# Kernel tuning notes

Hardware: AMD Instinct MI355X
Metric: run time of the kernel (lower is better)

## Reference

```python
import jax, jax.numpy as jnp
import numpy as np

B, N, T, D, H, E = 2, 1024, 8, 128, 4, 8192
DH = D // H
NEG_SLOPE = 0.2  # GATv2Conv default negative_slope


def _ln(x, g, b):
    m = jnp.mean(x, -1, keepdims=True)
    v = jnp.mean((x - m) ** 2, -1, keepdims=True)
    return (x - m) * jax.lax.rsqrt(v + 1e-5) * g + b


def _forward(x, edge_index, gat_wl, gat_wr, gat_att, gat_b, in_w, in_b, out_w, out_b,
             ffn_w1, ffn_b1, ffn_w2, ffn_b2, fus_w, fus_b,
             lns_g, lns_b, lnt1_g, lnt1_b, lnt2_g, lnt2_b, lnf_g, lnf_b):
    # ---- spatial branch: GATv2, vectorized over (B, T) instead of python loops ----
    loops = jnp.arange(N)
    src = jnp.concatenate([edge_index[0], loops])  # j: message source (PyG adds self loops)
    dst = jnp.concatenate([edge_index[1], loops])  # i: aggregation target
    xl = jnp.einsum('bntd,de->bnte', x, gat_wl).reshape(B, N, T, H, D)
    xr = jnp.einsum('bntd,de->bnte', x, gat_wr).reshape(B, N, T, H, D)
    ml = xl[:, src]                                  # [B,Et,T,H,D]
    mr = xr[:, dst]
    e = jax.nn.leaky_relu(ml + mr, NEG_SLOPE)
    logits = jnp.einsum('bethd,hd->beth', e, gat_att)
    logits = jnp.moveaxis(logits, 1, 0)              # [Et,B,T,H]
    mx = jax.ops.segment_max(logits, dst, num_segments=N)
    p = jnp.exp(logits - mx[dst])                    # stable edge softmax per dst node
    ssum = jax.ops.segment_sum(p, dst, num_segments=N)
    alpha = p / ssum[dst]                            # [Et,B,T,H]
    msg = alpha[..., None] * jnp.moveaxis(ml, 1, 0)
    agg = jax.ops.segment_sum(msg, dst, num_segments=N)  # [N,B,T,H,D]
    x_sp = jnp.moveaxis(agg.mean(3), 0, 1) + gat_b   # concat=False -> head mean; [B,N,T,D]
    x_sp = _ln(x_sp, lns_g, lns_b)

    # ---- temporal branch: MHA + FFN, vectorized over all B*N nodes ----
    xt = x.reshape(B * N, T, D)
    qkv = xt @ in_w + in_b
    q, k, v = jnp.split(qkv, 3, axis=-1)
    q = q.reshape(B * N, T, H, DH)
    k = k.reshape(B * N, T, H, DH)
    v = v.reshape(B * N, T, H, DH)
    scores = jnp.einsum('bthd,bshd->bhts', q, k) / np.float32(np.sqrt(DH))
    attn = jax.nn.softmax(scores, -1)
    o = jnp.einsum('bhts,bshd->bthd', attn, v).reshape(B * N, T, D)
    o = o @ out_w + out_b
    x1 = _ln(xt + o, lnt1_g, lnt1_b)
    ffn = jax.nn.gelu(x1 @ ffn_w1 + ffn_b1, approximate=False) @ ffn_w2 + ffn_b2
    x_tp = _ln(x1 + ffn, lnt2_g, lnt2_b).reshape(B, N, T, D)

    # ---- gated fusion with residual ----
    g = jax.nn.sigmoid(jnp.concatenate([x_sp, x_tp], -1) @ fus_w + fus_b)
    return _ln(g * x_sp + (1.0 - g) * x_tp + x, lnf_g, lnf_b)


def setup_inputs() -> dict:
    key = jax.random.key(0)
    ks = jax.random.split(key, 12)
    s = 0.05
    f = jnp.float32
    return {
        'x': jax.random.normal(ks[0], (B, N, T, D), f),
        'edge_index': jax.random.randint(ks[1], (2, E), 0, N),
        'gat_wl': jax.random.normal(ks[2], (D, H * D), f) * s,
        'gat_wr': jax.random.normal(ks[3], (D, H * D), f) * s,
        'gat_att': jax.random.normal(ks[4], (H, D), f) * s,
        'gat_b': jnp.zeros((D,), f),
        'in_w': jax.random.normal(ks[5], (D, 3 * D), f) * s,
        'in_b': jnp.zeros((3 * D,), f),
        'out_w': jax.random.normal(ks[6], (D, D), f) * s,
        'out_b': jnp.zeros((D,), f),
        'ffn_w1': jax.random.normal(ks[7], (D, 4 * D), f) * s,
        'ffn_b1': jnp.zeros((4 * D,), f),
        'ffn_w2': jax.random.normal(ks[8], (4 * D, D), f) * s,
        'ffn_b2': jnp.zeros((D,), f),
        'fus_w': jax.random.normal(ks[9], (2 * D, D), f) * s,
        'fus_b': jnp.zeros((D,), f),
        'lns_g': jnp.ones((D,), f), 'lns_b': jnp.zeros((D,), f),
        'lnt1_g': jnp.ones((D,), f), 'lnt1_b': jnp.zeros((D,), f),
        'lnt2_g': jnp.ones((D,), f), 'lnt2_b': jnp.zeros((D,), f),
        'lnf_g': jnp.ones((D,), f), 'lnf_b': jnp.zeros((D,), f),
    }


def reference(x, edge_index, gat_wl, gat_wr, gat_att, gat_b, in_w, in_b, out_w, out_b,
              ffn_w1, ffn_b1, ffn_w2, ffn_b2, fus_w, fus_b,
              lns_g, lns_b, lnt1_g, lnt1_b, lnt2_g, lnt2_b, lnf_g, lnf_b):
    return _forward(x, edge_index, gat_wl, gat_wr, gat_att, gat_b, in_w, in_b, out_w, out_b,
                    ffn_w1, ffn_b1, ffn_w2, ffn_b2, fus_w, fus_b,
                    lns_g, lns_b, lnt1_g, lnt1_b, lnt2_g, lnt2_b, lnf_g, lnf_b)
```

## Files before the change

kernel.cpp:

```cpp
#include <hip/hip_runtime.h>
#include <math.h>

#define B_ 2
#define N_ 1024
#define T_ 8
#define D_ 128
#define H_ 4
#define E_ 8192
#define EN_ 9216
#define M_ 16384

typedef unsigned short u16;
using bf16x8 = __attribute__((ext_vector_type(8))) short;
using f32x4  = __attribute__((ext_vector_type(4))) float;

__device__ __forceinline__ float bf2f(unsigned int u) {
  return __uint_as_float(u << 16);
}
__device__ __forceinline__ u16 f2bf(float f) {
  unsigned int x = __float_as_uint(f);
  x += 0x7fffu + ((x >> 16) & 1u);
  return (u16)(x >> 16);
}
__device__ __forceinline__ void load8f(const u16* p, float* f) {
  uint4 u = *(const uint4*)p;
  f[0]=bf2f(u.x & 0xffffu); f[1]=bf2f(u.x >> 16);
  f[2]=bf2f(u.y & 0xffffu); f[3]=bf2f(u.y >> 16);
  f[4]=bf2f(u.z & 0xffffu); f[5]=bf2f(u.z >> 16);
  f[6]=bf2f(u.w & 0xffffu); f[7]=bf2f(u.w >> 16);
}
__device__ __forceinline__ void unpack8(uint4 u, float* f) {
  f[0]=bf2f(u.x & 0xffffu); f[1]=bf2f(u.x >> 16);
  f[2]=bf2f(u.y & 0xffffu); f[3]=bf2f(u.y >> 16);
  f[4]=bf2f(u.z & 0xffffu); f[5]=bf2f(u.z >> 16);
  f[6]=bf2f(u.w & 0xffffu); f[7]=bf2f(u.w >> 16);
}
__device__ __forceinline__ void gl2lds(const u16* g, u16* l) {
  __builtin_amdgcn_global_load_lds(
      (const __attribute__((address_space(1))) unsigned int*)(const void*)g,
      (__attribute__((address_space(3))) unsigned int*)(void*)l,
      16, 0, 0);
}

__device__ __forceinline__ u16 conv_w_elem(int idx,
    const float* wl, const float* wr, const float* inw, const float* outw,
    const float* f1, const float* f2, const float* fw) {
  const float* src; int base, K, N;
  if      (idx < 65536)  { src = wl;   base = 0;      K = 128; N = 512; }
  else if (idx < 131072) { src = wr;   base = 65536;  K = 128; N = 512; }
  else if (idx < 180224) { src = inw;  base = 131072; K = 128; N = 384; }
  else if (idx < 196608) { src = outw; base = 180224; K = 128; N = 128; }
  else if (idx < 262144) { src = f1;   base = 196608; K = 128; N = 512; }
  else if (idx < 327680) { src = f2;   base = 262144; K = 512; N = 128; }
  else                   { src = fw;   base = 327680; K = 256; N = 128; }
  int o = idx - base;
  int n = o / K, k = o - n * K;
  return f2bf(src[k * N + n]);
}

__global__ __launch_bounds__(1024) void prep_csr_k(const float* __restrict__ x,
    const float* __restrict__ wl, const float* __restrict__ wr,
    const float* __restrict__ inw, const float* __restrict__ outw,
    const float* __restrict__ f1, const float* __restrict__ f2,
    const float* __restrict__ fw,
    u16* __restrict__ XB, u16* __restrict__ WB,
    const int* __restrict__ ei, int* __restrict__ offs, int* __restrict__ srcs) {
  __shared__ int cnt[N_];
  __shared__ int cur[N_];
  int bi = blockIdx.x;
  int tid = threadIdx.x;
  if (bi < 512) {
    int i = (bi * 1024 + tid) * 4;
    float4 v = *(const float4*)&x[i];
    u16 o[4] = {f2bf(v.x), f2bf(v.y), f2bf(v.z), f2bf(v.w)};
    *(ushort4*)&XB[i] = *(ushort4*)o;
    return;
  }
  if (bi < 600) {
    int base = (bi - 512) * 4096 + tid * 4;
#pragma unroll
    for (int j = 0; j < 4; ++j)
      WB[base + j] = conv_w_elem(base + j, wl, wr, inw, outw, f1, f2, fw);
    return;
  }
  cnt[tid] = 0;
  __syncthreads();
  for (int e = tid; e < EN_; e += 1024) {
    int d = (e < E_) ? ei[E_ + e] : (e - E_);
    atomicAdd(&cnt[d], 1);
  }
  __syncthreads();
  int mine = cnt[tid];
  for (int off = 1; off < 1024; off <<= 1) {
    int tv = (tid >= off) ? cnt[tid - off] : 0;
    __syncthreads();
    cnt[tid] += tv;
    __syncthreads();
  }
  int excl = cnt[tid] - mine;
  offs[tid] = excl;
  if (tid == 1023) offs[N_] = cnt[1023];
  cur[tid] = excl;
  __syncthreads();
  for (int e = tid; e < EN_; e += 1024) {
    int d = (e < E_) ? ei[E_ + e] : (e - E_);
    int s = (e < E_) ? ei[e] : (e - E_);
    int pos = atomicAdd(&cur[d], 1);
    srcs[pos] = s;
  }
}

template<int BM, int ACT, int ROUTE>
__global__ __launch_bounds__(256) void gemm_k(const u16* __restrict__ A, int lda,
                                              const u16* __restrict__ WT, int K,
                                              const float* __restrict__ bias,
                                              u16* __restrict__ C, int ldc,
                                              u16* __restrict__ R0,
                                              u16* __restrict__ R1,
                                              u16* __restrict__ R2,
                                              const float* __restrict__ b2) {
  constexpr int MI = BM / 32;
  __shared__ u16 As[BM * 32];
  __shared__ u16 Bs[128 * 32];
  int tid = threadIdx.x;
  int bx = blockIdx.x, by = blockIdx.y;
  int lane = tid & 63, wid = tid >> 6;
  int lr = lane & 15, lk = lane >> 4;
  int wm = (wid >> 1) * (BM / 2);
  int wn = (wid & 1) * 64;

  u16* Cb; int ldc_; int col0; const float* bias_;
  if (ROUTE) {
    if (bx < 4)      { Cb = R0; ldc_ = 512; col0 = bx * 128;       bias_ = nullptr; }
    else if (bx < 8) { Cb = R1; ldc_ = 512; col0 = (bx - 4) * 128; bias_ = nullptr; }
    else             { Cb = R2; ldc_ = 384; col0 = (bx - 8) * 128; bias_ = b2; }
  } else { Cb = C; ldc_ = ldc; col0 = bx * 128; bias_ = bias; }

  f32x4 acc[MI][4] = {};
  for (int k0 = 0; k0 < K; k0 += 32) {
    __syncthreads();
#pragma unroll
    for (int i = 0; i < BM / 64; ++i) {
      int o = tid * 16 + i * 4096;
      int row = o >> 6;
      int col = (o >> 1) & 31;
      gl2lds(A + (size_t)(by * BM + row) * lda + k0 + col,
             (u16*)((char*)As + wid * 1024 + i * 4096));
    }
#pragma unroll
    for (int i = 0; i < 2; ++i) {
      int o = tid * 16 + i * 4096;
      int nrow = o >> 6;
      int col = (o >> 1) & 31;
      gl2lds(WT + (size_t)(bx * 128 + nrow) * K + k0 + col,
             (u16*)((char*)Bs + wid * 1024 + i * 4096));
    }
    __syncthreads();
    bf16x8 bf[4];
#pragma unroll
    for (int ni = 0; ni < 4; ++ni)
      bf[ni] = *(const bf16x8*)&Bs[(wn + ni * 16 + lr) * 32 + lk * 8];
#pragma unroll
    for (int mi = 0; mi < MI; ++mi) {
      bf16x8 af = *(const bf16x8*)&As[(wm + mi * 16 + lr) * 32 + lk * 8];
#pragma unroll
      for (int ni = 0; ni < 4; ++ni)
        acc[mi][ni] = __builtin_amdgcn_mfma_f32_16x16x32_bf16(af, bf[ni], acc[mi][ni], 0, 0, 0);
    }
  }
  float bc[4];
#pragma unroll
  for (int ni = 0; ni < 4; ++ni)
    bc[ni] = bias_ ? bias_[col0 + wn + ni * 16 + lr] : 0.f;
#pragma unroll
  for (int mi = 0; mi < MI; ++mi) {
#pragma unroll
    for (int r = 0; r < 4; ++r) {
      int row = by * BM + wm + mi * 16 + lk * 4 + r;
#pragma unroll
      for (int ni = 0; ni < 4; ++ni) {
        int col = col0 + wn + ni * 16 + lr;
        float v = acc[mi][ni][r] + bc[ni];
        if (ACT) v = 0.5f * v * (1.f + erff(v * 0.70710678118f));
        Cb[(size_t)row * ldc_ + col] = f2bf(v);
      }
    }
  }
}

template<int EPI>
__global__ __launch_bounds__(256) void gemm_ln_k(const u16* __restrict__ A, int lda,
                                                 const u16* __restrict__ WT, int K,
                                                 const float* __restrict__ bias,
                                                 const float* __restrict__ xres,
                                                 const u16* __restrict__ xcat,
                                                 const float* __restrict__ lng,
                                                 const float* __restrict__ lnb,
                                                 float* __restrict__ o32,
                                                 u16* __restrict__ o16, int os16) {
  __shared__ u16 As[64 * 32];
  __shared__ u16 Bs[128 * 32];
  __shared__ float rs[64][2], rq[64][2];
  int tid = threadIdx.x;
  int by = blockIdx.y;
  int lane = tid & 63, wid = tid >> 6;
  int lr = lane & 15, lk = lane >> 4;
  int wm = (wid >> 1) * 32, wn = (wid & 1) * 64;

  f32x4 acc[2][4] = {};
  for (int k0 = 0; k0 < K; k0 += 32) {
    __syncthreads();
    {
      int o = tid * 16;
      int row = o >> 6;
      int col = (o >> 1) & 31;
      gl2lds(A + (size_t)(by * 64 + row) * lda + k0 + col,
             (u16*)((char*)As + wid * 1024));
    }
#pragma unroll
    for (int i = 0; i < 2; ++i) {
      int o = tid * 16 + i * 4096;
      int nrow = o >> 6;
      int col = (o >> 1) & 31;
      gl2lds(WT + (size_t)nrow * K + k0 + col,
             (u16*)((char*)Bs + wid * 1024 + i * 4096));
    }
    __syncthreads();
    bf16x8 bf[4];
#pragma unroll
    for (int ni = 0; ni < 4; ++ni)
      bf[ni] = *(const bf16x8*)&Bs[(wn + ni * 16 + lr) * 32 + lk * 8];
#pragma unroll
    for (int mi = 0; mi < 2; ++mi) {
      bf16x8 af = *(const bf16x8*)&As[(wm + mi * 16 + lr) * 32 + lk * 8];
#pragma unroll
      for (int ni = 0; ni < 4; ++ni)
        acc[mi][ni] = __builtin_amdgcn_mfma_f32_16x16x32_bf16(af, bf[ni], acc[mi][ni], 0, 0, 0);
    }
  }
  float bc[4];
#pragma unroll
  for (int ni = 0; ni < 4; ++ni) bc[ni] = bias[wn + ni * 16 + lr];

#pragma unroll
  for (int mi = 0; mi < 2; ++mi) {
#pragma unroll
    for (int r = 0; r < 4; ++r) {
      int row = by * 64 + wm + mi * 16 + lk * 4 + r;
      float s = 0.f, s2 = 0.f;
#pragma unroll
      for (int ni = 0; ni < 4; ++ni) {
        int col = wn + ni * 16 + lr;
        float v = acc[mi][ni][r] + bc[ni];
        if (EPI == 1 || EPI == 2) {
          v += xres[(size_t)row * 128 + col];
        } else {
          float gg = 1.f / (1.f + __expf(-v));
          float xsp = bf2f(xcat[(size_t)row * 256 + col]);
          float xtp = bf2f(xcat[(size_t)row * 256 + 128 + col]);
          v = gg * xsp + (1.f - gg) * xtp + xres[(size_t)row * 128 + col];
        }
        acc[mi][ni][r] = v;
        s += v; s2 += v * v;
      }
      s += __shfl_xor(s, 1, 64); s2 += __shfl_xor(s2, 1, 64);
      s += __shfl_xor(s, 2, 64); s2 += __shfl_xor(s2, 2, 64);
      s += __shfl_xor(s, 4, 64); s2 += __shfl_xor(s2, 4, 64);
      s += __shfl_xor(s, 8, 64); s2 += __shfl_xor(s2, 8, 64);
      if (lr == 0) {
        int rl = wm + mi * 16 + lk * 4 + r;
        rs[rl][wid & 1] = s;
        rq[rl][wid & 1] = s2;
      }
    }
  }
  __syncthreads();
#pragma unroll
  for (int mi = 0; mi < 2; ++mi) {
#pragma unroll
    for (int r = 0; r < 4; ++r) {
      int rl = wm + mi * 16 + lk * 4 + r;
      int row = by * 64 + rl;
      float tot = rs[rl][0] + rs[rl][1];
      float tq = rq[rl][0] + rq[rl][1];
      float mean = tot * (1.f / 128.f);
      float var = tq * (1.f / 128.f) - mean * mean;
      float rinv = rsqrtf(var + 1e-5f);
#pragma unroll
      for (int ni = 0; ni < 4; ++ni) {
        int col = wn + ni * 16 + lr;
        float o = (acc[mi][ni][r] - mean) * rinv * lng[col] + lnb[col];
        if (EPI != 2) o32[(size_t)row * 128 + col] = o;
        if (EPI != 3) o16[(size_t)row * os16 + col] = f2bf(o);
      }
    }
  }
}

__global__ __launch_bounds__(256) void gat_attn_k(const u16* __restrict__ XL,
                                                  const u16* __restrict__ XR,
                                                  const int* __restrict__ offs,
                                                  const int* __restrict__ srcs,
                                                  const float* __restrict__ att,
                                                  const float* __restrict__ gb,
                                                  const float* __restrict__ lng,
                                                  const float* __restrict__ lnb,
                                                  u16* __restrict__ XCAT,
                                                  const u16* __restrict__ QKV,
                                                  u16* __restrict__ OATT) {
  int bid = blockIdx.x;
  int wid = threadIdx.x >> 6;
  int lane = threadIdx.x & 63;
  if (bid < 4096) {
    int w = bid * 4 + wid;
    int n = w >> 4;
    int b = (w >> 3) & 1;
    int t = w & 7;
    int dd = (lane & 15) * 8;
    size_t tokn = (size_t)(b * N_ + n) * 8 + t;
    size_t rowoff = (size_t)b * (N_ * 8) + t;

    float mr[8], av[8];
    load8f(XR + tokn * 512 + lane * 8, mr);
    *(float4*)&av[0] = *(const float4*)(att + lane * 8);
    *(float4*)&av[4] = *(const float4*)(att + lane * 8 + 4);

    int beg = offs[n], end = offs[n + 1];
    float sH = 0.f;
    float acc[8] = {0.f, 0.f, 0.f, 0.f, 0.f, 0.f, 0.f, 0.f};
    int src0 = srcs[beg];
    uint4 raw_next = *(const uint4*)(XL + (rowoff + (size_t)src0 * 8) * 512 + lane * 8);
    for (int i = beg; i < end; ++i) {
      uint4 raw = raw_next;
      if (i + 1 < end) {
        int sn = srcs[i + 1];
        raw_next = *(const uint4*)(XL + (rowoff + (size_t)sn * 8) * 512 + lane * 8);
      }
      float ml[8];
      unpack8(raw, ml);
      float d = 0.f;
#pragma unroll
      for (int j = 0; j < 8; ++j) {
        float m = ml[j] + mr[j];
        m = fmaxf(m, 0.2f * m);
        d += m * av[j];
      }
      d += __shfl_xor(d, 1, 64);
      d += __shfl_xor(d, 2, 64);
      d += __shfl_xor(d, 4, 64);
      d += __shfl_xor(d, 8, 64);
      float p = __expf(d);
      sH += p;
#pragma unroll
      for (int j = 0; j < 8; ++j) acc[j] += p * ml[j];
    }
    float invS = 1.f / sH;
#pragma unroll
    for (int j = 0; j < 8; ++j) acc[j] *= invS;
#pragma unroll
    for (int j = 0; j < 8; ++j) {
      acc[j] += __shfl_xor(acc[j], 16, 64);
      acc[j] += __shfl_xor(acc[j], 32, 64);
    }
#pragma unroll
    for (int j = 0; j < 8; ++j) acc[j] = acc[j] * 0.25f + gb[dd + j];
    float s = 0.f, s2 = 0.f;
#pragma unroll
    for (int j = 0; j < 8; ++j) { s += acc[j]; s2 += acc[j] * acc[j]; }
#pragma unroll
    for (int m = 1; m < 16; m <<= 1) {
      s += __shfl_xor(s, m, 64);
      s2 += __shfl_xor(s2, m, 64);
    }
    float mean = s * (1.f / 128.f);
    float var = s2 * (1.f / 128.f) - mean * mean;
    float r = rsqrtf(var + 1e-5f);
    if (lane < 16) {
      u16 ob[8];
#pragma unroll
      for (int j = 0; j < 8; ++j)
        ob[j] = f2bf((acc[j] - mean) * r * lng[dd + j] + lnb[dd + j]);
      *(uint4*)&XCAT[tokn * 256 + dd] = *(uint4*)ob;
    }
    return;
  }
  int pair = (bid - 4096) * 4 + wid;
  int bn = pair >> 2, h = pair & 3;
  int t = lane >> 3, sidx = lane & 7;
  int dg = lane & 7;
  const u16* base = QKV + (size_t)bn * 8 * 384;
  float va[8][4];
#pragma unroll
  for (int s2 = 0; s2 < 8; ++s2) {
    ushort4 vv = *(const ushort4*)(base + s2 * 384 + 256 + h * 32 + dg * 4);
    va[s2][0] = bf2f(vv.x); va[s2][1] = bf2f(vv.y);
    va[s2][2] = bf2f(vv.z); va[s2][3] = bf2f(vv.w);
  }
  const u16* qp = base + t * 384 + h * 32;
  const u16* kp = base + sidx * 384 + 128 + h * 32;
  float sc = 0.f;
#pragma unroll
  for (int d0 = 0; d0 < 32; d0 += 8) {
    float q[8], k[8];
    load8f(qp + d0, q);
    load8f(kp + d0, k);
#pragma unroll
    for (int j = 0; j < 8; ++j) sc += q[j] * k[j];
  }
  sc *= 0.17677669529663687f;
  float m = sc;
  m = fmaxf(m, __shfl_xor(m, 1, 64));
  m = fmaxf(m, __shfl_xor(m, 2, 64));
  m = fmaxf(m, __shfl_xor(m, 4, 64));
  float p = __expf(sc - m);
  float S = p;
  S += __shfl_xor(S, 1, 64);
  S += __shfl_xor(S, 2, 64);
  S += __shfl_xor(S, 4, 64);
  float alpha = p / S;
  int tbase = lane & 56;
  float o0 = 0.f, o1 = 0.f, o2 = 0.f, o3 = 0.f;
#pragma unroll
  for (int s2 = 0; s2 < 8; ++s2) {
    float a = __shfl(alpha, tbase + s2, 64);
    o0 += a * va[s2][0];
    o1 += a * va[s2][1];
    o2 += a * va[s2][2];
    o3 += a * va[s2][3];
  }
  u16 ov[4] = {f2bf(o0), f2bf(o1), f2bf(o2), f2bf(o3)};
  *(ushort4*)&OATT[((size_t)bn * 8 + t) * 128 + h * 32 + dg * 4] = *(ushort4*)ov;
}

extern "C" void kernel_launch(void* const* d_in, const int* in_sizes, int n_in,
                              void* d_out, int out_size, void* d_ws, size_t ws_size,
                              hipStream_t stream) {
  const float* x       = (const float*)d_in[0];
  const int*   ei      = (const int*)d_in[1];
  const float* gat_att = (const float*)d_in[4];
  const float* gat_b   = (const float*)d_in[5];
  const float* in_b    = (const float*)d_in[7];
  const float* out_b   = (const float*)d_in[9];
  const float* ffn_b1  = (const float*)d_in[11];
  const float* ffn_b2  = (const float*)d_in[13];
  const float* fus_b   = (const float*)d_in[15];
  const float* lns_g   = (const float*)d_in[16];
  const float* lns_b   = (const float*)d_in[17];
  const float* lnt1_g  = (const float*)d_in[18];
  const float* lnt1_b  = (const float*)d_in[19];
  const float* lnt2_g  = (const float*)d_in[20];
  const float* lnt2_b  = (const float*)d_in[21];
  const float* lnf_g   = (const float*)d_in[22];
  const float* lnf_b   = (const float*)d_in[23];

  char* ws = (char*)d_ws;
  u16*   WB    = (u16*)ws;
  u16*   WT1   = WB;
  u16*   WTO   = WB + 180224;
  u16*   WTF1  = WB + 196608;
  u16*   WTF2  = WB + 262144;
  u16*   WTFUS = WB + 327680;
  int*   OFFS  = (int*)(ws + 3145728);
  int*   SRCS  = (int*)(ws + 3153920);
  u16*   XB   = (u16*)(ws + 4194304);
  u16*   OATT = XB;
  u16*   XL   = (u16*)(ws + 8388608);
  u16*   FFNH = XL;
  u16*   XR   = (u16*)(ws + 25165824);
  float* X1   = (float*)(ws + 33554432);
  u16*   QKV  = (u16*)(ws + 41943040);
  u16*   X1B  = (u16*)(ws + 41943040);
  u16*   XCAT = (u16*)(ws + 62914560);

  prep_csr_k<<<dim3(601), dim3(1024), 0, stream>>>(x,
      (const float*)d_in[2], (const float*)d_in[3], (const float*)d_in[6],
      (const float*)d_in[8], (const float*)d_in[10], (const float*)d_in[12],
      (const float*)d_in[14], XB, WB, ei, OFFS, SRCS);

  gemm_k<128,0,1><<<dim3(11, 128), dim3(256), 0, stream>>>(
      XB, 128, WT1, 128, nullptr, nullptr, 0, XL, XR, QKV, in_b);

  gat_attn_k<<<dim3(6144), dim3(256), 0, stream>>>(XL, XR, OFFS, SRCS,
      gat_att, gat_b, lns_g, lns_b, XCAT, QKV, OATT);

  gemm_ln_k<1><<<dim3(1, 256), dim3(256), 0, stream>>>(
      OATT, 128, WTO, 128, out_b, x, nullptr, lnt1_g, lnt1_b, X1, X1B, 128);

  gemm_k<128,1,0><<<dim3(4, 128), dim3(256), 0, stream>>>(
      X1B, 128, WTF1, 128, ffn_b1, FFNH, 512, nullptr, nullptr, nullptr, nullptr);

  gemm_ln_k<2><<<dim3(1, 256), dim3(256), 0, stream>>>(
      FFNH, 512, WTF2, 512, ffn_b2, X1, nullptr, lnt2_g, lnt2_b,
      nullptr, XCAT + 128, 256);

  gemm_ln_k<3><<<dim3(1, 256), dim3(256), 0, stream>>>(
      XCAT, 256, WTFUS, 256, fus_b, x, XCAT, lnf_g, lnf_b,
      (float*)d_out, nullptr, 0);
}
```

Baseline: 223.2 us.

## Fuse all stages into one persistent kernel with software grid barriers

Replaces seven separate kernel launches with a single persistent kernel of 768 blocks that loops over virtual tiles for each stage and separates stages with atomic-counter grid barriers. The aim is to remove launch overhead and inter-kernel gaps between the short stages. In exchange, it relies on all 768 blocks being co-resident (launch bounds of 3 blocks per CU), which risks deadlock if occupancy is lower. It also adds barrier spin cost and does CSR construction in a single 256-thread block.

```diff
diff --git a/kernel.cpp b/kernel.cpp
--- a/kernel.cpp
+++ b/kernel.cpp
@@ -9,6 +9,7 @@
 #define E_ 8192
 #define EN_ 9216
 #define M_ 16384
+#define G_ 768
 
 typedef unsigned short u16;
 using bf16x8 = __attribute__((ext_vector_type(8))) short;
@@ -40,6 +41,17 @@
       (const __attribute__((address_space(1))) unsigned int*)(const void*)g,
       (__attribute__((address_space(3))) unsigned int*)(void*)l,
       16, 0, 0);
+}
+
+__device__ __forceinline__ void gridbar(int* bar, int idx) {
+  __syncthreads();
+  if (threadIdx.x == 0) {
+    __threadfence();
+    atomicAdd(&bar[idx], 1);
+    while (atomicAdd(&bar[idx], 0) < G_) __builtin_amdgcn_s_sleep(1);
+    __threadfence();
+  }
+  __syncthreads();
 }
 
 __device__ __forceinline__ u16 conv_w_elem(int idx,
@@ -58,72 +70,13 @@
   return f2bf(src[k * N + n]);
 }
 
-__global__ __launch_bounds__(1024) void prep_csr_k(const float* __restrict__ x,
-    const float* __restrict__ wl, const float* __restrict__ wr,
-    const float* __restrict__ inw, const float* __restrict__ outw,
-    const float* __restrict__ f1, const float* __restrict__ f2,
-    const float* __restrict__ fw,
-    u16* __restrict__ XB, u16* __restrict__ WB,
-    const int* __restrict__ ei, int* __restrict__ offs, int* __restrict__ srcs) {
-  __shared__ int cnt[N_];
-  __shared__ int cur[N_];
-  int bi = blockIdx.x;
+template<int BM, int ACT, int ROUTE>
+__device__ __forceinline__ void gemm_tile(int bx, int by,
+    const u16* A, int lda, const u16* WT, int K, const float* bias,
+    u16* C, int ldc, u16* R0, u16* R1, u16* R2, const float* b2,
+    u16* As, u16* Bs) {
+  constexpr int MI = BM / 32;
   int tid = threadIdx.x;
-  if (bi < 512) {
-    int i = (bi * 1024 + tid) * 4;
-    float4 v = *(const float4*)&x[i];
-    u16 o[4] = {f2bf(v.x), f2bf(v.y), f2bf(v.z), f2bf(v.w)};
-    *(ushort4*)&XB[i] = *(ushort4*)o;
-    return;
-  }
-  if (bi < 600) {
-    int base = (bi - 512) * 4096 + tid * 4;
-#pragma unroll
-    for (int j = 0; j < 4; ++j)
-      WB[base + j] = conv_w_elem(base + j, wl, wr, inw, outw, f1, f2, fw);
-    return;
-  }
-  cnt[tid] = 0;
-  __syncthreads();
-  for (int e = tid; e < EN_; e += 1024) {
-    int d = (e < E_) ? ei[E_ + e] : (e - E_);
-    atomicAdd(&cnt[d], 1);
-  }
-  __syncthreads();
-  int mine = cnt[tid];
-  for (int off = 1; off < 1024; off <<= 1) {
-    int tv = (tid >= off) ? cnt[tid - off] : 0;
-    __syncthreads();
-    cnt[tid] += tv;
-    __syncthreads();
-  }
-  int excl = cnt[tid] - mine;
-  offs[tid] = excl;
-  if (tid == 1023) offs[N_] = cnt[1023];
-  cur[tid] = excl;
-  __syncthreads();
-  for (int e = tid; e < EN_; e += 1024) {
-    int d = (e < E_) ? ei[E_ + e] : (e - E_);
-    int s = (e < E_) ? ei[e] : (e - E_);
-    int pos = atomicAdd(&cur[d], 1);
-    srcs[pos] = s;
-  }
-}
-
-template<int BM, int ACT, int ROUTE>
-__global__ __launch_bounds__(256) void gemm_k(const u16* __restrict__ A, int lda,
-                                              const u16* __restrict__ WT, int K,
-                                              const float* __restrict__ bias,
-                                              u16* __restrict__ C, int ldc,
-                                              u16* __restrict__ R0,
-                                              u16* __restrict__ R1,
-                                              u16* __restrict__ R2,
-                                              const float* __restrict__ b2) {
-  constexpr int MI = BM / 32;
-  __shared__ u16 As[BM * 32];
-  __shared__ u16 Bs[128 * 32];
-  int tid = threadIdx.x;
-  int bx = blockIdx.x, by = blockIdx.y;
   int lane = tid & 63, wid = tid >> 6;
   int lr = lane & 15, lk = lane >> 4;
   int wm = (wid >> 1) * (BM / 2);
@@ -189,20 +142,12 @@
 }
 
 template<int EPI>
-__global__ __launch_bounds__(256) void gemm_ln_k(const u16* __restrict__ A, int lda,
-                                                 const u16* __restrict__ WT, int K,
-                                                 const float* __restrict__ bias,
-                                                 const float* __restrict__ xres,
-                                                 const u16* __restrict__ xcat,
-                                                 const float* __restrict__ lng,
-                                                 const float* __restrict__ lnb,
-                                                 float* __restrict__ o32,
-                                                 u16* __restrict__ o16, int os16) {
-  __shared__ u16 As[64 * 32];
-  __shared__ u16 Bs[128 * 32];
-  __shared__ float rs[64][2], rq[64][2];
+__device__ __forceinline__ void gemm_ln_tile(int by,
+    const u16* A, int lda, const u16* WT, int K, const float* bias,
+    const float* xres, const u16* xcat, const float* lng, const float* lnb,
+    float* o32, u16* o16, int os16,
+    u16* As, u16* Bs, float* rs, float* rq) {
   int tid = threadIdx.x;
-  int by = blockIdx.y;
   int lane = tid & 63, wid = tid >> 6;
   int lr = lane & 15, lk = lane >> 4;
   int wm = (wid >> 1) * 32, wn = (wid & 1) * 64;
@@ -269,8 +214,8 @@
       s += __shfl_xor(s, 8, 64); s2 += __shfl_xor(s2, 8, 64);
       if (lr == 0) {
         int rl = wm + mi * 16 + lk * 4 + r;
-        rs[rl][wid & 1] = s;
-        rq[rl][wid & 1] = s2;
+        rs[rl * 2 + (wid & 1)] = s;
+        rq[rl * 2 + (wid & 1)] = s2;
       }
     }
   }
@@ -281,8 +226,8 @@
     for (int r = 0; r < 4; ++r) {
       int rl = wm + mi * 16 + lk * 4 + r;
       int row = by * 64 + rl;
-      float tot = rs[rl][0] + rs[rl][1];
-      float tq = rq[rl][0] + rq[rl][1];
+      float tot = rs[rl * 2] + rs[rl * 2 + 1];
+      float tq = rq[rl * 2] + rq[rl * 2 + 1];
       float mean = tot * (1.f / 128.f);
       float var = tq * (1.f / 128.f) - mean * mean;
       float rinv = rsqrtf(var + 1e-5f);
@@ -295,96 +240,86 @@
       }
     }
   }
-}
-
-__global__ __launch_bounds__(256) void gat_attn_k(const u16* __restrict__ XL,
-                                                  const u16* __restrict__ XR,
-                                                  const int* __restrict__ offs,
-                                                  const int* __restrict__ srcs,
-                                                  const float* __restrict__ att,
-                                                  const float* __restrict__ gb,
-                                                  const float* __restrict__ lng,
-                                                  const float* __restrict__ lnb,
-                                                  u16* __restrict__ XCAT,
-                                                  const u16* __restrict__ QKV,
-                                                  u16* __restrict__ OATT) {
-  int bid = blockIdx.x;
-  int wid = threadIdx.x >> 6;
-  int lane = threadIdx.x & 63;
-  if (bid < 4096) {
-    int w = bid * 4 + wid;
-    int n = w >> 4;
-    int b = (w >> 3) & 1;
-    int t = w & 7;
-    int dd = (lane & 15) * 8;
-    size_t tokn = (size_t)(b * N_ + n) * 8 + t;
-    size_t rowoff = (size_t)b * (N_ * 8) + t;
-
-    float mr[8], av[8];
-    load8f(XR + tokn * 512 + lane * 8, mr);
-    *(float4*)&av[0] = *(const float4*)(att + lane * 8);
-    *(float4*)&av[4] = *(const float4*)(att + lane * 8 + 4);
-
-    int beg = offs[n], end = offs[n + 1];
-    float sH = 0.f;
-    float acc[8] = {0.f, 0.f, 0.f, 0.f, 0.f, 0.f, 0.f, 0.f};
-    int src0 = srcs[beg];
-    uint4 raw_next = *(const uint4*)(XL + (rowoff + (size_t)src0 * 8) * 512 + lane * 8);
-    for (int i = beg; i < end; ++i) {
-      uint4 raw = raw_next;
-      if (i + 1 < end) {
-        int sn = srcs[i + 1];
-        raw_next = *(const uint4*)(XL + (rowoff + (size_t)sn * 8) * 512 + lane * 8);
-      }
-      float ml[8];
-      unpack8(raw, ml);
-      float d = 0.f;
-#pragma unroll
-      for (int j = 0; j < 8; ++j) {
-        float m = ml[j] + mr[j];
-        m = fmaxf(m, 0.2f * m);
-        d += m * av[j];
-      }
-      d += __shfl_xor(d, 1, 64);
-      d += __shfl_xor(d, 2, 64);
-      d += __shfl_xor(d, 4, 64);
-      d += __shfl_xor(d, 8, 64);
-      float p = __expf(d);
-      sH += p;
-#pragma unroll
-      for (int j = 0; j < 8; ++j) acc[j] += p * ml[j];
-    }
-    float invS = 1.f / sH;
-#pragma unroll
-    for (int j = 0; j < 8; ++j) acc[j] *= invS;
+  __syncthreads();
+}
+
+__device__ __forceinline__ void gat_wave(int w, int lane,
+    const u16* XL, const u16* XR, const int* offs, const int* srcs,
+    const float* att, const float* gb, const float* lng, const float* lnb,
+    u16* XCAT) {
+  int n = w >> 4;
+  int b = (w >> 3) & 1;
+  int t = w & 7;
+  int dd = (lane & 15) * 8;
+  size_t tokn = (size_t)(b * N_ + n) * 8 + t;
+  size_t rowoff = (size_t)b * (N_ * 8) + t;
+
+  float mr[8], av[8];
+  load8f(XR + tokn * 512 + lane * 8, mr);
+  *(float4*)&av[0] = *(const float4*)(att + lane * 8);
+  *(float4*)&av[4] = *(const float4*)(att + lane * 8 + 4);
+
+  int beg = offs[n], end = offs[n + 1];
+  float sH = 0.f;
+  float acc[8] = {0.f, 0.f, 0.f, 0.f, 0.f, 0.f, 0.f, 0.f};
+  int src0 = srcs[beg];
+  uint4 raw_next = *(const uint4*)(XL + (rowoff + (size_t)src0 * 8) * 512 + lane * 8);
+  for (int i = beg; i < end; ++i) {
+    uint4 raw = raw_next;
+    if (i + 1 < end) {
+      int sn = srcs[i + 1];
+      raw_next = *(const uint4*)(XL + (rowoff + (size_t)sn * 8) * 512 + lane * 8);
+    }
+    float ml[8];
+    unpack8(raw, ml);
+    float d = 0.f;
 #pragma unroll
     for (int j = 0; j < 8; ++j) {
-      acc[j] += __shfl_xor(acc[j], 16, 64);
-      acc[j] += __shfl_xor(acc[j], 32, 64);
-    }
-#pragma unroll
-    for (int j = 0; j < 8; ++j) acc[j] = acc[j] * 0.25f + gb[dd + j];
-    float s = 0.f, s2 = 0.f;
-#pragma unroll
-    for (int j = 0; j < 8; ++j) { s += acc[j]; s2 += acc[j] * acc[j]; }
-#pragma unroll
-    for (int m = 1; m < 16; m <<= 1) {
-      s += __shfl_xor(s, m, 64);
-      s2 += __shfl_xor(s2, m, 64);
-    }
-    float mean = s * (1.f / 128.f);
-    float var = s2 * (1.f / 128.f) - mean * mean;
-    float r = rsqrtf(var + 1e-5f);
-    if (lane < 16) {
-      u16 ob[8];
-#pragma unroll
-      for (int j = 0; j < 8; ++j)
-        ob[j] = f2bf((acc[j] - mean) * r * lng[dd + j] + lnb[dd + j]);
-      *(uint4*)&XCAT[tokn * 256 + dd] = *(uint4*)ob;
-    }
-    return;
-  }
-  int pair = (bid - 4096) * 4 + wid;
+      float m = ml[j] + mr[j];
+      m = fmaxf(m, 0.2f * m);
+      d += m * av[j];
+    }
+    d += __shfl_xor(d, 1, 64);
+    d += __shfl_xor(d, 2, 64);
+    d += __shfl_xor(d, 4, 64);
+    d += __shfl_xor(d, 8, 64);
+    float p = __expf(d);
+    sH += p;
+#pragma unroll
+    for (int j = 0; j < 8; ++j) acc[j] += p * ml[j];
+  }
+  float invS = 1.f / sH;
+#pragma unroll
+  for (int j = 0; j < 8; ++j) acc[j] *= invS;
+#pragma unroll
+  for (int j = 0; j < 8; ++j) {
+    acc[j] += __shfl_xor(acc[j], 16, 64);
+    acc[j] += __shfl_xor(acc[j], 32, 64);
+  }
+#pragma unroll
+  for (int j = 0; j < 8; ++j) acc[j] = acc[j] * 0.25f + gb[dd + j];
+  float s = 0.f, s2 = 0.f;
+#pragma unroll
+  for (int j = 0; j < 8; ++j) { s += acc[j]; s2 += acc[j] * acc[j]; }
+#pragma unroll
+  for (int m = 1; m < 16; m <<= 1) {
+    s += __shfl_xor(s, m, 64);
+    s2 += __shfl_xor(s2, m, 64);
+  }
+  float mean = s * (1.f / 128.f);
+  float var = s2 * (1.f / 128.f) - mean * mean;
+  float r = rsqrtf(var + 1e-5f);
+  if (lane < 16) {
+    u16 ob[8];
+#pragma unroll
+    for (int j = 0; j < 8; ++j)
+      ob[j] = f2bf((acc[j] - mean) * r * lng[dd + j] + lnb[dd + j]);
+    *(uint4*)&XCAT[tokn * 256 + dd] = *(uint4*)ob;
+  }
+}
+
+__device__ __forceinline__ void attn_wave(int pair, int lane,
+    const u16* QKV, u16* OATT) {
   int bn = pair >> 2, h = pair & 3;
   int t = lane >> 3, sidx = lane & 7;
   int dg = lane & 7;
@@ -432,36 +367,138 @@
   *(ushort4*)&OATT[((size_t)bn * 8 + t) * 128 + h * 32 + dg * 4] = *(ushort4*)ov;
 }
 
+__global__ __launch_bounds__(256, 3) void mega_k(
+    const float* __restrict__ x, const int* __restrict__ ei,
+    const float* __restrict__ wl, const float* __restrict__ wr,
+    const float* __restrict__ inw, const float* __restrict__ outw,
+    const float* __restrict__ f1, const float* __restrict__ f2,
+    const float* __restrict__ fwp,
+    const float* __restrict__ gat_att, const float* __restrict__ gat_b,
+    const float* __restrict__ in_b, const float* __restrict__ out_b,
+    const float* __restrict__ ffn_b1, const float* __restrict__ ffn_b2,
+    const float* __restrict__ fus_b,
+    const float* __restrict__ lns_g, const float* __restrict__ lns_b,
+    const float* __restrict__ lnt1_g, const float* __restrict__ lnt1_b,
+    const float* __restrict__ lnt2_g, const float* __restrict__ lnt2_b,
+    const float* __restrict__ lnf_g, const float* __restrict__ lnf_b,
+    u16* __restrict__ XB, u16* __restrict__ WB,
+    int* __restrict__ OFFS, int* __restrict__ SRCS,
+    u16* __restrict__ XL, u16* __restrict__ XR, u16* __restrict__ QKV,
+    u16* __restrict__ OATT, float* __restrict__ X1, u16* __restrict__ X1B,
+    u16* __restrict__ FFNH, u16* __restrict__ XCAT,
+    float* __restrict__ out, int* __restrict__ bar) {
+  __shared__ char smem[17408];
+  u16* As = (u16*)smem;
+  u16* Bs = (u16*)(smem + 8192);
+  float* rs = (float*)(smem + 16384);
+  float* rq = rs + 128;
+
+  int bid = blockIdx.x;
+  int tid = threadIdx.x;
+  int wid = tid >> 6, lane = tid & 63;
+
+  u16* WTO   = WB + 180224;
+  u16* WTF1  = WB + 196608;
+  u16* WTF2  = WB + 262144;
+  u16* WTFUS = WB + 327680;
+
+  if (bid == 0) {
+    int* cnt = (int*)smem;
+    int* cur = cnt + 1024;
+    int* ps  = (int*)(smem + 8192);
+    for (int i = tid; i < N_; i += 256) cnt[i] = 0;
+    __syncthreads();
+    for (int e = tid; e < EN_; e += 256) {
+      int d = (e < E_) ? ei[E_ + e] : (e - E_);
+      atomicAdd(&cnt[d], 1);
+    }
+    __syncthreads();
+    int c0 = cnt[tid * 4], c1 = cnt[tid * 4 + 1];
+    int c2 = cnt[tid * 4 + 2], c3 = cnt[tid * 4 + 3];
+    int sum4 = c0 + c1 + c2 + c3;
+    ps[tid] = sum4;
+    __syncthreads();
+    for (int off = 1; off < 256; off <<= 1) {
+      int v = (tid >= off) ? ps[tid - off] : 0;
+      __syncthreads();
+      ps[tid] += v;
+      __syncthreads();
+    }
+    int base = ps[tid] - sum4;
+    int o0 = base, o1 = base + c0, o2 = base + c0 + c1, o3 = base + c0 + c1 + c2;
+    cur[tid * 4] = o0; cur[tid * 4 + 1] = o1;
+    cur[tid * 4 + 2] = o2; cur[tid * 4 + 3] = o3;
+    OFFS[tid * 4] = o0; OFFS[tid * 4 + 1] = o1;
+    OFFS[tid * 4 + 2] = o2; OFFS[tid * 4 + 3] = o3;
+    if (tid == 255) OFFS[N_] = ps[255];
+    __syncthreads();
+    for (int e = tid; e < EN_; e += 256) {
+      int d = (e < E_) ? ei[E_ + e] : (e - E_);
+      int s = (e < E_) ? ei[e] : (e - E_);
+      int pos = atomicAdd(&cur[d], 1);
+      SRCS[pos] = s;
+    }
+  } else {
+    for (int i = (bid - 1) * 256 + tid; i < 524288; i += (G_ - 1) * 256) {
+      float4 v = *(const float4*)&x[i * 4];
+      u16 o[4] = {f2bf(v.x), f2bf(v.y), f2bf(v.z), f2bf(v.w)};
+      *(ushort4*)&XB[i * 4] = *(ushort4*)o;
+    }
+    for (int i = (bid - 1) * 256 + tid; i < 90112; i += (G_ - 1) * 256) {
+      int base = i * 4;
+#pragma unroll
+      for (int j = 0; j < 4; ++j)
+        WB[base + j] = conv_w_elem(base + j, wl, wr, inw, outw, f1, f2, fwp);
+    }
+  }
+  gridbar(bar, 0);
+
+  for (int vb = bid; vb < 1408; vb += G_) {
+    int bx = vb >> 7, by = vb & 127;
+    gemm_tile<128, 0, 1>(bx, by, XB, 128, WB, 128, nullptr, nullptr, 0,
+                         XL, XR, QKV, in_b, As, Bs);
+  }
+  gridbar(bar, 1);
+
+  for (int vb = bid; vb < 6144; vb += G_) {
+    if (vb < 4096)
+      gat_wave(vb * 4 + wid, lane, XL, XR, OFFS, SRCS, gat_att, gat_b,
+               lns_g, lns_b, XCAT);
+    else
+      attn_wave((vb - 4096) * 4 + wid, lane, QKV, OATT);
+  }
+  gridbar(bar, 2);
+
+  for (int vb = bid; vb < 256; vb += G_)
+    gemm_ln_tile<1>(vb, OATT, 128, WTO, 128, out_b, x, nullptr,
+                    lnt1_g, lnt1_b, X1, X1B, 128, As, Bs, rs, rq);
+  gridbar(bar, 3);
+
+  for (int vb = bid; vb < 512; vb += G_) {
+    int bx = vb >> 7, by = vb & 127;
+    gemm_tile<128, 1, 0>(bx, by, X1B, 128, WTF1, 128, ffn_b1, FFNH, 512,
+                         nullptr, nullptr, nullptr, nullptr, As, Bs);
+  }
+  gridbar(bar, 4);
+
+  for (int vb = bid; vb < 256; vb += G_)
+    gemm_ln_tile<2>(vb, FFNH, 512, WTF2, 512, ffn_b2, X1, nullptr,
+                    lnt2_g, lnt2_b, nullptr, XCAT + 128, 256, As, Bs, rs, rq);
+  gridbar(bar, 5);
+
+  for (int vb = bid; vb < 256; vb += G_)
+    gemm_ln_tile<3>(vb, XCAT, 256, WTFUS, 256, fus_b, x, XCAT,
+                    lnf_g, lnf_b, out, nullptr, 0, As, Bs, rs, rq);
+}
+
 extern "C" void kernel_launch(void* const* d_in, const int* in_sizes, int n_in,
                               void* d_out, int out_size, void* d_ws, size_t ws_size,
                               hipStream_t stream) {
-  const float* x       = (const float*)d_in[0];
-  const int*   ei      = (const int*)d_in[1];
-  const float* gat_att = (const float*)d_in[4];
-  const float* gat_b   = (const float*)d_in[5];
-  const float* in_b    = (const float*)d_in[7];
-  const float* out_b   = (const float*)d_in[9];
-  const float* ffn_b1  = (const float*)d_in[11];
-  const float* ffn_b2  = (const float*)d_in[13];
-  const float* fus_b   = (const float*)d_in[15];
-  const float* lns_g   = (const float*)d_in[16];
-  const float* lns_b   = (const float*)d_in[17];
-  const float* lnt1_g  = (const float*)d_in[18];
-  const float* lnt1_b  = (const float*)d_in[19];
-  const float* lnt2_g  = (const float*)d_in[20];
-  const float* lnt2_b  = (const float*)d_in[21];
-  const float* lnf_g   = (const float*)d_in[22];
-  const float* lnf_b   = (const float*)d_in[23];
-
   char* ws = (char*)d_ws;
-  u16*   WB    = (u16*)ws;
-  u16*   WT1   = WB;
-  u16*   WTO   = WB + 180224;
-  u16*   WTF1  = WB + 196608;
-  u16*   WTF2  = WB + 262144;
-  u16*   WTFUS = WB + 327680;
-  int*   OFFS  = (int*)(ws + 3145728);
-  int*   SRCS  = (int*)(ws + 3153920);
+  u16*   WB   = (u16*)ws;
+  int*   OFFS = (int*)(ws + 3145728);
+  int*   SRCS = (int*)(ws + 3153920);
+  int*   BAR  = (int*)(ws + 3190784);
   u16*   XB   = (u16*)(ws + 4194304);
   u16*   OATT = XB;
   u16*   XL   = (u16*)(ws + 8388608);
@@ -472,28 +509,21 @@
   u16*   X1B  = (u16*)(ws + 41943040);
   u16*   XCAT = (u16*)(ws + 62914560);
 
-  prep_csr_k<<<dim3(601), dim3(1024), 0, stream>>>(x,
+  hipMemsetAsync(BAR, 0, 32, stream);
+
+  mega_k<<<dim3(G_), dim3(256), 0, stream>>>(
+      (const float*)d_in[0], (const int*)d_in[1],
       (const float*)d_in[2], (const float*)d_in[3], (const float*)d_in[6],
       (const float*)d_in[8], (const float*)d_in[10], (const float*)d_in[12],
-      (const float*)d_in[14], XB, WB, ei, OFFS, SRCS);
-
-  gemm_k<128,0,1><<<dim3(11, 128), dim3(256), 0, stream>>>(
-      XB, 128, WT1, 128, nullptr, nullptr, 0, XL, XR, QKV, in_b);
-
-  gat_attn_k<<<dim3(6144), dim3(256), 0, stream>>>(XL, XR, OFFS, SRCS,
-      gat_att, gat_b, lns_g, lns_b, XCAT, QKV, OATT);
-
-  gemm_ln_k<1><<<dim3(1, 256), dim3(256), 0, stream>>>(
-      OATT, 128, WTO, 128, out_b, x, nullptr, lnt1_g, lnt1_b, X1, X1B, 128);
-
-  gemm_k<128,1,0><<<dim3(4, 128), dim3(256), 0, stream>>>(
-      X1B, 128, WTF1, 128, ffn_b1, FFNH, 512, nullptr, nullptr, nullptr, nullptr);
-
-  gemm_ln_k<2><<<dim3(1, 256), dim3(256), 0, stream>>>(
-      FFNH, 512, WTF2, 512, ffn_b2, X1, nullptr, lnt2_g, lnt2_b,
-      nullptr, XCAT + 128, 256);
-
-  gemm_ln_k<3><<<dim3(1, 256), dim3(256), 0, stream>>>(
-      XCAT, 256, WTFUS, 256, fus_b, x, XCAT, lnf_g, lnf_b,
-      (float*)d_out, nullptr, 0);
-}
+      (const float*)d_in[14],
+      (const float*)d_in[4], (const float*)d_in[5],
+      (const float*)d_in[7], (const float*)d_in[9],
+      (const float*)d_in[11], (const float*)d_in[13],
+      (const float*)d_in[15],
+      (const float*)d_in[16], (const float*)d_in[17],
+      (const float*)d_in[18], (const float*)d_in[19],
+      (const float*)d_in[20], (const float*)d_in[21],
+      (const float*)d_in[22], (const float*)d_in[23],
+      XB, WB, OFFS, SRCS, XL, XR, QKV, OATT, X1, X1B, FFNH, XCAT,
+      (float*)d_out, BAR);
+}
```

Result: slower. 753.6 us (+237.6%).
